# Kernel tuning notes

Hardware: AMD Instinct MI355X
Metric: run time of the kernel (lower is better)

Reference implementation:

```python
import jax, jax.numpy as jnp
import numpy as np

T, B, K = 512, 1024, 48            # time steps, batch, tagset size
START, STOP = K - 2, K - 1         # tag_to_ix[START_TAG], tag_to_ix[STOP_TAG]
NEG = -10000.0


def setup_inputs() -> dict:
    key = jax.random.key(0)
    k1, k2, k3, k4 = jax.random.split(key, 4)
    # post-tanh emission features (output of tanh(hidden2tag(...))), time-major [T,B,K]
    feats = jnp.tanh(jax.random.normal(k1, (T, B, K), dtype=jnp.float32))
    transitions = jax.random.normal(k2, (K, K), dtype=jnp.float32)
    # CRF structural constraints, same as torch init:
    transitions = transitions.at[START, :].set(NEG).at[:, STOP].set(NEG)
    tags = jax.random.randint(k3, (B, T), 0, K - 2)       # gold tags exclude START/STOP
    lengths = jax.random.randint(k4, (B,), 1, T + 1)      # valid sequence lengths
    return {"feats": feats, "transitions": transitions, "tags": tags, "lengths": lengths}


def _crf_loss(feats, transitions, tags, lengths):
    Tn, Bn, Kn = feats.shape
    mask = jnp.arange(Tn)[:, None] < lengths[None, :]            # [T,B] valid-token mask

    # ---- forward algorithm (logZ) ----
    alpha0 = jnp.full((Bn, Kn), NEG, dtype=feats.dtype).at[:, START].set(0.0)

    def step(alpha, x):
        feat_t, m_t = x                                          # [B,K], [B]
        # scores[b, next, prev] = alpha[b,prev] + trans[next,prev] + emit[b,next]
        scores = alpha[:, None, :] + transitions[None, :, :] + feat_t[:, :, None]
        new_alpha = jax.nn.logsumexp(scores, axis=2)             # [B,K]
        alpha = jnp.where(m_t[:, None], new_alpha, alpha)        # freeze finished seqs
        return alpha, None

    alpha, _ = jax.lax.scan(step, alpha0, (feats, mask))
    log_z = jax.nn.logsumexp(alpha + transitions[STOP][None, :], axis=1)  # [B]

    # ---- gold path score ----
    tags_ext = jnp.concatenate(
        [jnp.full((Bn, 1), START, dtype=tags.dtype), tags], axis=1)       # [B,T+1]
    prev_t = tags_ext[:, :-1]                                             # [B,T]
    next_t = tags_ext[:, 1:]                                              # [B,T]
    feats_bt = feats.transpose(1, 0, 2)                                   # [B,T,K]
    emit = jnp.take_along_axis(feats_bt, next_t[:, :, None], axis=2)[:, :, 0]  # [B,T]
    trans_s = transitions[next_t, prev_t]                                 # [B,T]
    gold = jnp.sum(jnp.where(mask.T, trans_s + emit, 0.0), axis=1)        # [B]
    last_tag = jnp.take_along_axis(tags_ext, lengths[:, None], axis=1)[:, 0]
    gold = gold + transitions[STOP, last_tag]

    return jnp.sum(log_z - gold)


def reference(feats, transitions, tags, lengths):
    return _crf_loss(feats, transitions, tags, lengths)
```

## Files before the change

### kernel.cpp

```cpp
#include <hip/hip_runtime.h>
#include <math.h>

#define T_LEN 512
#define B_N   1024
#define K_N   48
#define START_TAG (K_N - 2)
#define STOP_TAG  (K_N - 1)
#define NEG   -10000.0f


using f32x2 = __attribute__((ext_vector_type(2))) float;

__device__ __forceinline__ float bcast(float v, int k) {
    return __uint_as_float(__builtin_amdgcn_readlane(__float_as_uint(v), k));
}

__device__ __forceinline__ float matvec46(const f32x2 (&E2)[23], float src) {
    const int qb = __float_as_int(src);
    f32x2 a0 = {0.f, 0.f}, a1 = {0.f, 0.f}, a2 = {0.f, 0.f}, a3 = {0.f, 0.f};
#define PKFMA(P, ACC) { \
        const unsigned int lo = (unsigned int)__builtin_amdgcn_readlane(qb, 2*(P)); \
        const unsigned int hi = (unsigned int)__builtin_amdgcn_readlane(qb, 2*(P)+1); \
        const unsigned long long sp = ((unsigned long long)hi << 32) | lo; \
        asm("v_pk_fma_f32 %0, %1, %2, %0" : "+v"(ACC) : "v"(E2[P]), "s"(sp)); }
    PKFMA(0,a0)  PKFMA(1,a1)  PKFMA(2,a2)  PKFMA(3,a3)
    PKFMA(4,a0)  PKFMA(5,a1)  PKFMA(6,a2)  PKFMA(7,a3)
    PKFMA(8,a0)  PKFMA(9,a1)  PKFMA(10,a2) PKFMA(11,a3)
    PKFMA(12,a0) PKFMA(13,a1) PKFMA(14,a2) PKFMA(15,a3)
    PKFMA(16,a0) PKFMA(17,a1) PKFMA(18,a2) PKFMA(19,a3)
    PKFMA(20,a0) PKFMA(21,a1) PKFMA(22,a2)
#undef PKFMA
    const f32x2 s = (a0 + a1) + (a2 + a3);
    return s.x + s.y;
}

__device__ __forceinline__ void renorm(float& q, float& C) {
    const float g = bcast(q, 0);
    C += __logf(g);
    q *= __builtin_amdgcn_rcpf(g);
}

template <int BWD>
__device__ __forceinline__ void run_chain(const float* __restrict__ fb,
                                          int rbase,
                                          const f32x2 (&E2)[23],
                                          int steps, int lane_c,
                                          float& q, float& C)
{
    const size_t sT = (size_t)B_N * K_N;
    auto row_of = [&](int i) -> int {
        int r = BWD ? (rbase - i) : (rbase + i);
        r = (r < 0) ? 0 : r;
        r = (r > T_LEN - 1) ? (T_LEN - 1) : r;
        return r;
    };
    auto step = [&](bool on, float fv) {
        if (BWD) {
            const float u = q * __expf(fv);
            const float w = matvec46(E2, u);
            q = on ? w : q;
        } else {
            const float w = matvec46(E2, q);
            q = on ? w * __expf(fv) : q;
        }
    };

    float f0[8], f1[8];
    #pragma unroll
    for (int i = 0; i < 8; ++i)
        f0[i] = fb[(size_t)row_of(i) * sT + lane_c];

    const int nfull = steps >> 4;
    #pragma unroll 1
    for (int blk = 0; blk < nfull; ++blk) {
        const int t0 = blk * 16;
        #pragma unroll
        for (int i = 0; i < 8; ++i)
            f1[i] = fb[(size_t)row_of(t0 + 8 + i) * sT + lane_c];
        #pragma unroll
        for (int i = 0; i < 8; ++i) {
            step(true, f0[i]);
            if (i == 3 || i == 7) renorm(q, C);
        }
        #pragma unroll
        for (int i = 0; i < 8; ++i)
            f0[i] = fb[(size_t)row_of(t0 + 16 + i) * sT + lane_c];
        #pragma unroll
        for (int i = 0; i < 8; ++i) {
            step(true, f1[i]);
            if (i == 3 || i == 7) renorm(q, C);
        }
    }
    const int rem = steps & 15;
    if (rem) {
        const int t0 = nfull * 16;
        #pragma unroll
        for (int i = 0; i < 8; ++i)
            f1[i] = fb[(size_t)row_of(t0 + 8 + i) * sT + lane_c];
        #pragma unroll
        for (int i = 0; i < 8; ++i) {
            step(i < rem, f0[i]);
            if (i == 3 || i == 7) renorm(q, C);
        }
        #pragma unroll
        for (int i = 0; i < 8; ++i) {
            step(8 + i < rem, f1[i]);
            if (i == 3 || i == 7) renorm(q, C);
        }
    }
}

__global__ __launch_bounds__(1024)
void lpt_sort_kernel(const int* __restrict__ lengths, int* __restrict__ perm)
{
    __shared__ int hist[512];
    __shared__ int offs[512];
    const int tid = threadIdx.x;
    if (tid < 512) hist[tid] = 0;
    __syncthreads();
    const int len = lengths[tid];
    const int key = 512 - len;
    atomicAdd(&hist[key], 1);
    __syncthreads();
    if (tid < 512) offs[tid] = hist[tid];
    __syncthreads();
    for (int d = 1; d < 512; d <<= 1) {
        int v = 0;
        if (tid < 512 && tid >= d) v = offs[tid - d];
        __syncthreads();
        if (tid < 512) offs[tid] += v;
        __syncthreads();
    }
    const int p = atomicSub(&offs[key], 1) - 1;
    perm[p] = tid;
}

__global__ __launch_bounds__(128)
__attribute__((amdgpu_waves_per_eu(1, 1)))
void crf_fused_kernel(
    const float* __restrict__ feats,
    const float* __restrict__ trans,
    const int*   __restrict__ tags,
    const int*   __restrict__ lengths,
    const int*   __restrict__ perm,
    float* __restrict__ out)
{
    const int b      = perm[blockIdx.x];
    const int tid    = threadIdx.x;
    const int lane   = tid & 63;
    const int wid    = tid >> 6;
    const int len    = lengths[b];
    const int lm1    = len - 1;
    const int m      = (len + 1) >> 1;
    const int lane_c = (lane < K_N) ? lane : (K_N - 1);

    __shared__ __attribute__((aligned(16))) float sh_p[64];
    __shared__ float sh_cb;
    __shared__ float sh_gold;

    const float* fb = feats + (size_t)b * K_N;
    const size_t sT = (size_t)B_N * K_N;

    f32x2 E2[23];
    if (wid == 0) {
        const float* tr = trans + lane_c * K_N;
        #pragma unroll
        for (int p = 0; p < 23; ++p) {
            E2[p].x = __expf(tr[2 * p]);
            E2[p].y = __expf(tr[2 * p + 1]);
        }
    } else {
        #pragma unroll
        for (int p = 0; p < 23; ++p) {
            E2[p].x = __expf(trans[(2 * p) * K_N + lane_c]);
            E2[p].y = __expf(trans[(2 * p + 1) * K_N + lane_c]);
        }
    }

    float q, C = 0.0f;
    int   steps;
    if (wid == 0) {
        q = __expf(trans[lane_c * K_N + START_TAG] + fb[lane_c]);
        steps = m - 1;
        run_chain<0>(fb, 1, E2, steps, lane_c, q, C);
    } else {
        q = __expf(trans[STOP_TAG * K_N + lane_c]);
        steps = len - m;
        run_chain<1>(fb, lm1, E2, steps, lane_c, q, C);
    }
    renorm(q, C);

    if (wid == 1) {
        float gsum = 0.0f;
        for (int t = lane; t < len; t += 64) {
            int next = tags[(size_t)b * T_LEN + t];
            int prev = (t == 0) ? START_TAG : tags[(size_t)b * T_LEN + t - 1];
            gsum += trans[next * K_N + prev] + fb[(size_t)t * sT + next];
        }
        #pragma unroll
        for (int off = 32; off >= 1; off >>= 1)
            gsum += __shfl_xor(gsum, off);

        sh_p[lane] = q;
        if (lane == 0) {
            sh_cb = C;
            int last = tags[(size_t)b * T_LEN + len - 1];
            sh_gold = gsum + trans[STOP_TAG * K_N + last];
        }
    }
    __syncthreads();

    if (wid == 0) {
        float term = (lane < K_N) ? q * sh_p[lane] : 0.0f;
        #pragma unroll
        for (int off = 32; off >= 1; off >>= 1)
            term += __shfl_xor(term, off);
        if (lane == 0) {
            float log_z = C + sh_cb + __logf(term);
            atomicAdd(out, log_z - sh_gold);
        }
    }
}

extern "C" void kernel_launch(void* const* d_in, const int* in_sizes, int n_in,
                              void* d_out, int out_size, void* d_ws, size_t ws_size,
                              hipStream_t stream) {
    const float* feats   = (const float*)d_in[0];
    const float* trans   = (const float*)d_in[1];
    const int*   tags    = (const int*)d_in[2];
    const int*   lengths = (const int*)d_in[3];
    float* out = (float*)d_out;
    int*   perm = (int*)d_ws;

    hipMemsetAsync(out, 0, sizeof(float) * out_size, stream);
    lpt_sort_kernel<<<1, B_N, 0, stream>>>(lengths, perm);
    crf_fused_kernel<<<B_N, 128, 0, stream>>>(feats, trans, tags, lengths, perm, out);
}
```

Before: 192.2 us.

## Renormalize every step, fold rcp into emission factor, prefetch exp'd feats

Replaces the periodic renorm calls (every 4 steps, each with a dependent readlane, log and multiply on q) with a per-step normalization. Each step reads q[0], takes its reciprocal, folds that into the already-exponentiated emission, and accumulates log2(g) off the critical path, converting to natural log at the end. The exp of the features moves into the prefetch loads so it is off the serial chain, and the tail skips the second half-block when it is not needed. In exchange every step now carries a readlane+rcp+log2, which could lengthen the dependency chain per step.

```diff
diff --git a/kernel.cpp b/kernel.cpp
--- a/kernel.cpp
+++ b/kernel.cpp
@@ -45,7 +45,7 @@
                                           int rbase,
                                           const f32x2 (&E2)[23],
                                           int steps, int lane_c,
-                                          float& q, float& C)
+                                          float& q, float& C2)
 {
     const size_t sT = (size_t)B_N * K_N;
     auto row_of = [&](int i) -> int {
@@ -54,21 +54,24 @@
         r = (r > T_LEN - 1) ? (T_LEN - 1) : r;
         return r;
     };
-    auto step = [&](bool on, float fv) {
+    auto step = [&](bool on, float ef) {
+        const float g = bcast(q, 0);
+        const float r = __builtin_amdgcn_rcpf(g);
         if (BWD) {
-            const float u = q * __expf(fv);
+            const float u = q * (ef * r);
             const float w = matvec46(E2, u);
             q = on ? w : q;
         } else {
             const float w = matvec46(E2, q);
-            q = on ? w * __expf(fv) : q;
-        }
+            q = on ? w * (ef * r) : q;
+        }
+        C2 += on ? __builtin_amdgcn_logf(g) : 0.0f;
     };
 
     float f0[8], f1[8];
     #pragma unroll
     for (int i = 0; i < 8; ++i)
-        f0[i] = fb[(size_t)row_of(i) * sT + lane_c];
+        f0[i] = __expf(fb[(size_t)row_of(i) * sT + lane_c]);
 
     const int nfull = steps >> 4;
     #pragma unroll 1
@@ -76,36 +79,30 @@
         const int t0 = blk * 16;
         #pragma unroll
         for (int i = 0; i < 8; ++i)
-            f1[i] = fb[(size_t)row_of(t0 + 8 + i) * sT + lane_c];
-        #pragma unroll
-        for (int i = 0; i < 8; ++i) {
+            f1[i] = __expf(fb[(size_t)row_of(t0 + 8 + i) * sT + lane_c]);
+        #pragma unroll
+        for (int i = 0; i < 8; ++i)
             step(true, f0[i]);
-            if (i == 3 || i == 7) renorm(q, C);
-        }
-        #pragma unroll
-        for (int i = 0; i < 8; ++i)
-            f0[i] = fb[(size_t)row_of(t0 + 16 + i) * sT + lane_c];
-        #pragma unroll
-        for (int i = 0; i < 8; ++i) {
+        #pragma unroll
+        for (int i = 0; i < 8; ++i)
+            f0[i] = __expf(fb[(size_t)row_of(t0 + 16 + i) * sT + lane_c]);
+        #pragma unroll
+        for (int i = 0; i < 8; ++i)
             step(true, f1[i]);
-            if (i == 3 || i == 7) renorm(q, C);
-        }
     }
     const int rem = steps & 15;
     if (rem) {
         const int t0 = nfull * 16;
         #pragma unroll
         for (int i = 0; i < 8; ++i)
-            f1[i] = fb[(size_t)row_of(t0 + 8 + i) * sT + lane_c];
-        #pragma unroll
-        for (int i = 0; i < 8; ++i) {
+            f1[i] = __expf(fb[(size_t)row_of(t0 + 8 + i) * sT + lane_c]);
+        #pragma unroll
+        for (int i = 0; i < 8; ++i)
             step(i < rem, f0[i]);
-            if (i == 3 || i == 7) renorm(q, C);
-        }
-        #pragma unroll
-        for (int i = 0; i < 8; ++i) {
-            step(8 + i < rem, f1[i]);
-            if (i == 3 || i == 7) renorm(q, C);
+        if (rem > 8) {
+            #pragma unroll
+            for (int i = 0; i < 8; ++i)
+                step(8 + i < rem, f1[i]);
         }
     }
 }
@@ -177,17 +174,15 @@
         }
     }
 
-    float q, C = 0.0f;
-    int   steps;
+    float q, C2 = 0.0f, C = 0.0f;
     if (wid == 0) {
         q = __expf(trans[lane_c * K_N + START_TAG] + fb[lane_c]);
-        steps = m - 1;
-        run_chain<0>(fb, 1, E2, steps, lane_c, q, C);
+        run_chain<0>(fb, 1, E2, m - 1, lane_c, q, C2);
     } else {
         q = __expf(trans[STOP_TAG * K_N + lane_c]);
-        steps = len - m;
-        run_chain<1>(fb, lm1, E2, steps, lane_c, q, C);
-    }
+        run_chain<1>(fb, lm1, E2, len - m, lane_c, q, C2);
+    }
+    C = C2 * 0.6931471805599453f;
     renorm(q, C);
 
     if (wid == 1) {
```

After: 197.6 us. 1.03x slower.
